# Kernel tuning notes

Hardware: AMD Instinct MI355X
Metric: run time of the kernel (lower is better)

The kernel has to match this reference:

```python
import jax, jax.numpy as jnp
import numpy as np

B, D, H, Wd = 256, 15, 63, 126  # batch, depth, lat, lon
K = 5                            # kernel == stride (reduce_resolution)
PD, PH, PW = 0, 1, 2             # ZeroPadding3D sizes
OD, OH, OW = (D + 2 * PD) // K, (H + 2 * PH) // K, (Wd + 2 * PW) // K  # 3,13,26


def setup_inputs() -> dict:
    key = jax.random.key(0)
    k1, k2, k3, k4 = jax.random.split(key, 4)
    x = jax.random.normal(k1, (B, D, H, Wd, 1), dtype=jnp.float32)
    # binary ocean mask: 1 = ocean (kept), 0 = land (removed)
    land = (jax.random.uniform(k2, (D, H, Wd, 1)) > 0.25).astype(jnp.float32)
    # positive cell volumes
    volumes = jax.random.uniform(k3, (D, H, Wd, 1), dtype=jnp.float32) + 0.5
    # per-location (non-shared) locally-connected weights
    W = jax.random.normal(k4, (OD, OH, OW, K, K, K, 1, 1), dtype=jnp.float32) / np.sqrt(K ** 3)
    b = jnp.zeros((OD, OH, OW, 1), dtype=jnp.float32)
    return {"x": x, "land": land, "volumes": volumes, "W": W, "b": b}


def reference(x, land, volumes, W, b):
    # LandValueRemoval3D (start): zero out land cells
    h = x * land
    # ZeroPadding3D((0,1,2))
    h = jnp.pad(h, ((0, 0), (0, 0), (PH, PH), (PW, PW), (0, 0)))
    # LocallyConnected3D, kernel==stride==5: non-overlapping blocks -> blocked einsum
    # (B, OD, K, OH, K, OW, K, C)
    hb = h.reshape(B, OD, K, OH, K, OW, K, 1)
    y = jnp.einsum('bipjqkrc,ijkpqrcf->bijkf', hb, W) + b  # per-location weights
    y = jax.nn.relu(y)
    # UpSampling3D((5,5,5))
    y = jnp.repeat(jnp.repeat(jnp.repeat(y, K, axis=1), K, axis=2), K, axis=3)
    # Cropping3D((0,1,2))
    y = y[:, :, PH:-PH, PW:-PW, :]
    # LandValueRemoval3D (end)
    y = y * land
    # MassConversation3D: rescale so total mass (x * volume) is conserved per sample
    mass_in = jnp.sum(x * volumes, axis=(1, 2, 3, 4), keepdims=True)
    mass_out = jnp.sum(y * volumes, axis=(1, 2, 3, 4), keepdims=True)
    return y * (mass_in / mass_out)
```

## Files before the change

### kernel.cpp

```cpp
#include <hip/hip_runtime.h>

#define BATCH 256
#define DD 15
#define HH 63
#define WW 126
#define OD 3
#define OH 13
#define OWI 26
#define SPAT (DD*HH*WW)
#define HWSZ (HH*WW)
#define NBLK (OD*OH*OWI)
#define IJB  (OH*OWI)
#define WEXP_D (65*130)
#define NWEXP (DD*WEXP_D)
#define NGRP 16

__global__ __launch_bounds__(256)
void prep_kernel(const float* __restrict__ W, const float* __restrict__ land,
                 const float* __restrict__ vols,
                 float* __restrict__ Wexp, float* __restrict__ lv,
                 unsigned short* __restrict__ tbl) {
    int idx = blockIdx.x * 256 + threadIdx.x;
    if (idx < NWEXP) {
        int d   = idx / WEXP_D;
        int rem = idx - d * WEXP_D;
        int hp1 = rem / 130;
        int wp  = rem - hp1 * 130;
        float val = 0.f;
        if (hp1 >= 1 && hp1 <= HH && wp >= 2 && wp < 128) {
            int i = d / 5, p = d - 5 * i;
            int h = hp1 - 1, w = wp - 2;
            int j = hp1 / 5, q = hp1 - 5 * j;
            int k = wp / 5,  r = wp - 5 * k;
            int blk = (i * OH + j) * OWI + k;
            val = W[blk * 125 + p * 25 + q * 5 + r] * land[(d * HH + h) * WW + w];
        }
        Wexp[idx] = val;
    } else if (idx < NWEXP + NBLK) {
        int blk = idx - NWEXP;
        int ij = blk / OWI, k = blk - ij * OWI;
        int i  = ij / OH,   j = ij - i * OH;
        float s = 0.f;
        for (int p = 0; p < 5; ++p) {
            int d = i * 5 + p;
            for (int q = 0; q < 5; ++q) {
                int h = j * 5 + q - 1;
                if ((unsigned)h >= (unsigned)HH) continue;
                int base = (d * HH + h) * WW;
                for (int r = 0; r < 5; ++r) {
                    int w = k * 5 + r - 2;
                    if ((unsigned)w < (unsigned)WW)
                        s += land[base + w] * vols[base + w];
                }
            }
        }
        lv[blk] = s;
    } else if (idx < NWEXP + NBLK + SPAT) {
        int r  = idx - NWEXP - NBLK;
        int d  = r / HWSZ;
        int r2 = r - d * HWSZ;
        int h  = r2 / WW;
        int w  = r2 - h * WW;
        tbl[r] = (unsigned short)(((d / 5) * OH + (h + 1) / 5) * OWI + (w + 2) / 5);
    }
}

__global__ __launch_bounds__(512)
void conv_kernel(const float* __restrict__ x, const float* __restrict__ vols,
                 const float* __restrict__ Wexp, const float* __restrict__ lv,
                 const float* __restrict__ bias, float* __restrict__ y_small,
                 double* __restrict__ mass_in, double* __restrict__ mass_out) {
    __shared__ float acc[NGRP * IJB];
    __shared__ float redmi[8];
    __shared__ float redmo[8];
    const int tid  = threadIdx.x;
    const int wv   = tid >> 6;
    const int lane = tid & 63;
    const int lg   = lane & 31;
    const int g    = wv * 2 + (lane >> 5);
    const int b    = blockIdx.x / OD;
    const int i    = blockIdx.x - b * OD;

    for (int t = tid; t < NGRP * IJB; t += 512) acc[t] = 0.f;
    __syncthreads();

    float mi = 0.f;
    if (lg < OWI) {
        const int wbase = 5 * lg - 2;
        const float* xb = x + (size_t)b * SPAT + i * 5 * HWSZ;
        const float* vb = vols + i * 5 * HWSZ;
        const float* wb = Wexp + i * 5 * WEXP_D;
        float* accw = acc + g * IJB + lg;
        for (int rr = g; rr < 5 * HH; rr += NGRP) {
            const int p = rr / HH;
            const int h = rr - p * HH;
            const float* xrow = xb + p * HWSZ + h * WW;
            const float* vrow = vb + p * HWSZ + h * WW;
            const float* wrow = wb + p * WEXP_D + (h + 1) * 130 + 5 * lg;
            float s = 0.f;
            #pragma unroll
            for (int r = 0; r < 5; ++r) {
                const int w = wbase + r;
                if ((unsigned)w < (unsigned)WW) {
                    const float xv = xrow[w];
                    s  = fmaf(xv, wrow[r], s);
                    mi = fmaf(xv, vrow[w], mi);
                }
            }
            accw[((h + 1) / 5) * OWI] += s;
        }
    }
    #pragma unroll
    for (int s2 = 32; s2; s2 >>= 1) mi += __shfl_down(mi, s2, 64);
    if (lane == 0) redmi[wv] = mi;
    __syncthreads();

    float mo = 0.f;
    if (tid < IJB) {
        float v = 0.f;
        #pragma unroll
        for (int w2 = 0; w2 < NGRP; ++w2) v += acc[w2 * IJB + tid];
        const int blk = i * IJB + tid;
        const float y = fmaxf(v + bias[blk], 0.f);
        y_small[(size_t)b * NBLK + blk] = y;
        mo = y * lv[blk];
    }
    #pragma unroll
    for (int s2 = 32; s2; s2 >>= 1) mo += __shfl_down(mo, s2, 64);
    if (lane == 0) redmo[wv] = mo;
    __syncthreads();
    if (tid == 0) {
        float tmi = 0.f, tmo = 0.f;
        #pragma unroll
        for (int w2 = 0; w2 < 8; ++w2) { tmi += redmi[w2]; tmo += redmo[w2]; }
        atomicAdd(mass_in  + b, (double)tmi);
        atomicAdd(mass_out + b, (double)tmo);
    }
}

__global__ void scale_kernel(const double* __restrict__ mi,
                             const double* __restrict__ mo,
                             float* __restrict__ s) {
    int t = threadIdx.x;
    if (t < BATCH) s[t] = (float)(mi[t] / mo[t]);
}

__global__ __launch_bounds__(256)
void out_kernel(const float* __restrict__ y, const unsigned short* __restrict__ tbl,
                const float* __restrict__ land, const float* __restrict__ scale,
                float4* __restrict__ out) {
    const unsigned PAIR4 = (2u * SPAT) / 4u;
    const unsigned CH    = 3721u;
    const unsigned b2    = blockIdx.x >> 4;
    const unsigned chunk = blockIdx.x & 15u;
    const unsigned begin = chunk * CH;
    const unsigned end   = (begin + CH < PAIR4) ? begin + CH : PAIR4;
    const float s0 = scale[2 * b2], s1 = scale[2 * b2 + 1];
    const float* y0 = y + (size_t)(2 * b2) * NBLK;
    const float* y1 = y0 + NBLK;
    const unsigned base4 = b2 * PAIR4;

    for (unsigned t = begin + threadIdx.x; t < end; t += 256) {
        const unsigned e0 = t * 4u;
        float o[4];
        #pragma unroll
        for (int up = 0; up < 2; ++up) {
            const unsigned e  = e0 + 2u * up;
            const unsigned bo = e >= (unsigned)SPAT;
            const unsigned r  = e - (bo ? (unsigned)SPAT : 0u);
            const unsigned tt = *reinterpret_cast<const unsigned*>(tbl + r);
            const float2   l2 = *reinterpret_cast<const float2*>(land + r);
            const float* yb = bo ? y1 : y0;
            const float  sc = bo ? s1 : s0;
            o[2 * up]     = yb[tt & 0xFFFFu] * l2.x * sc;
            o[2 * up + 1] = yb[tt >> 16]     * l2.y * sc;
        }
        out[base4 + t] = make_float4(o[0], o[1], o[2], o[3]);
    }
}

extern "C" void kernel_launch(void* const* d_in, const int* in_sizes, int n_in,
                              void* d_out, int out_size, void* d_ws, size_t ws_size,
                              hipStream_t stream) {
    const float* x    = (const float*)d_in[0];
    const float* land = (const float*)d_in[1];
    const float* vols = (const float*)d_in[2];
    const float* Wt   = (const float*)d_in[3];
    const float* bias = (const float*)d_in[4];

    char* ws = (char*)d_ws;
    double*         mass_in  = (double*)(ws);
    double*         mass_out = (double*)(ws + 2048);
    float*          scale    = (float*) (ws + 4096);
    float*          Wexp     = (float*) (ws + 5120);
    float*          lv       = (float*) (ws + 512120);
    unsigned short* tbl      = (unsigned short*)(ws + 516176);
    float*          y_small  = (float*) (ws + 754320);

    hipMemsetAsync(ws, 0, 4096, stream);

    prep_kernel<<<(NWEXP + NBLK + SPAT + 255) / 256, 256, 0, stream>>>(
        Wt, land, vols, Wexp, lv, tbl);

    conv_kernel<<<BATCH * OD, 512, 0, stream>>>(
        x, vols, Wexp, lv, bias, y_small, mass_in, mass_out);

    scale_kernel<<<1, 256, 0, stream>>>(mass_in, mass_out, scale);

    out_kernel<<<128 * 16, 256, 0, stream>>>(
        y_small, tbl, land, scale, (float4*)d_out);
}
```

Before: 340.4 us.

## Unroll conv rows by four, stage scaled y in LDS, use nontemporal output stores

```diff
diff --git a/kernel.cpp b/kernel.cpp
--- a/kernel.cpp
+++ b/kernel.cpp
@@ -14,6 +14,9 @@
 #define WEXP_D (65*130)
 #define NWEXP (DD*WEXP_D)
 #define NGRP 16
+#define NROWS (5*HH)
+
+typedef float f32x4 __attribute__((ext_vector_type(4)));
 
 __global__ __launch_bounds__(256)
 void prep_kernel(const float* __restrict__ W, const float* __restrict__ land,
@@ -84,32 +87,70 @@
     for (int t = tid; t < NGRP * IJB; t += 512) acc[t] = 0.f;
     __syncthreads();
 
-    float mi = 0.f;
+    float miv[4] = {0.f, 0.f, 0.f, 0.f};
     if (lg < OWI) {
         const int wbase = 5 * lg - 2;
         const float* xb = x + (size_t)b * SPAT + i * 5 * HWSZ;
         const float* vb = vols + i * 5 * HWSZ;
-        const float* wb = Wexp + i * 5 * WEXP_D;
-        float* accw = acc + g * IJB + lg;
-        for (int rr = g; rr < 5 * HH; rr += NGRP) {
+        const float* wb = Wexp + i * 5 * WEXP_D + 5 * lg;
+        float* accg = acc + g * IJB + lg;
+
+        const int start = 20 * g;
+        const int end   = (start + 20 < NROWS) ? start + 20 : NROWS;
+
+        int rr = start;
+        for (; rr + 3 < end; rr += 4) {
+            float s[4];
+            #pragma unroll
+            for (int u = 0; u < 4; ++u) {
+                const int row = rr + u;
+                const int p = row / HH;
+                const int h = row - p * HH;
+                const float* xrow = xb + p * HWSZ + h * WW;
+                const float* vrow = vb + p * HWSZ + h * WW;
+                const float* wrow = wb + p * WEXP_D + (h + 1) * 130;
+                float sv = 0.f;
+                float mv = miv[u];
+                #pragma unroll
+                for (int r = 0; r < 5; ++r) {
+                    const int w = wbase + r;
+                    if ((unsigned)w < (unsigned)WW) {
+                        const float xv = xrow[w];
+                        sv = fmaf(xv, wrow[r], sv);
+                        mv = fmaf(xv, vrow[w], mv);
+                    }
+                }
+                miv[u] = mv;
+                s[u] = sv;
+            }
+            #pragma unroll
+            for (int u = 0; u < 4; ++u) {
+                const int row = rr + u;
+                const int p = row / HH;
+                const int h = row - p * HH;
+                accg[((h + 1) / 5) * OWI] += s[u];
+            }
+        }
+        for (; rr < end; ++rr) {
             const int p = rr / HH;
             const int h = rr - p * HH;
             const float* xrow = xb + p * HWSZ + h * WW;
             const float* vrow = vb + p * HWSZ + h * WW;
-            const float* wrow = wb + p * WEXP_D + (h + 1) * 130 + 5 * lg;
-            float s = 0.f;
+            const float* wrow = wb + p * WEXP_D + (h + 1) * 130;
+            float sv = 0.f;
             #pragma unroll
             for (int r = 0; r < 5; ++r) {
                 const int w = wbase + r;
                 if ((unsigned)w < (unsigned)WW) {
                     const float xv = xrow[w];
-                    s  = fmaf(xv, wrow[r], s);
-                    mi = fmaf(xv, vrow[w], mi);
+                    sv     = fmaf(xv, wrow[r], sv);
+                    miv[0] = fmaf(xv, vrow[w], miv[0]);
                 }
             }
-            accw[((h + 1) / 5) * OWI] += s;
-        }
-    }
+            accg[((h + 1) / 5) * OWI] += sv;
+        }
+    }
+    float mi = (miv[0] + miv[1]) + (miv[2] + miv[3]);
     #pragma unroll
     for (int s2 = 32; s2; s2 >>= 1) mi += __shfl_down(mi, s2, 64);
     if (lane == 0) redmi[wv] = mi;
@@ -148,7 +189,8 @@
 __global__ __launch_bounds__(256)
 void out_kernel(const float* __restrict__ y, const unsigned short* __restrict__ tbl,
                 const float* __restrict__ land, const float* __restrict__ scale,
-                float4* __restrict__ out) {
+                f32x4* __restrict__ out) {
+    __shared__ float ylds[2 * NBLK];
     const unsigned PAIR4 = (2u * SPAT) / 4u;
     const unsigned CH    = 3721u;
     const unsigned b2    = blockIdx.x >> 4;
@@ -156,10 +198,12 @@
     const unsigned begin = chunk * CH;
     const unsigned end   = (begin + CH < PAIR4) ? begin + CH : PAIR4;
     const float s0 = scale[2 * b2], s1 = scale[2 * b2 + 1];
-    const float* y0 = y + (size_t)(2 * b2) * NBLK;
-    const float* y1 = y0 + NBLK;
+    const float* yb = y + (size_t)(2 * b2) * NBLK;
+    for (int t = threadIdx.x; t < 2 * NBLK; t += 256)
+        ylds[t] = yb[t] * (t < NBLK ? s0 : s1);
+    __syncthreads();
+
     const unsigned base4 = b2 * PAIR4;
-
     for (unsigned t = begin + threadIdx.x; t < end; t += 256) {
         const unsigned e0 = t * 4u;
         float o[4];
@@ -170,12 +214,13 @@
             const unsigned r  = e - (bo ? (unsigned)SPAT : 0u);
             const unsigned tt = *reinterpret_cast<const unsigned*>(tbl + r);
             const float2   l2 = *reinterpret_cast<const float2*>(land + r);
-            const float* yb = bo ? y1 : y0;
-            const float  sc = bo ? s1 : s0;
-            o[2 * up]     = yb[tt & 0xFFFFu] * l2.x * sc;
-            o[2 * up + 1] = yb[tt >> 16]     * l2.y * sc;
-        }
-        out[base4 + t] = make_float4(o[0], o[1], o[2], o[3]);
+            const unsigned yo = bo ? (unsigned)NBLK : 0u;
+            o[2 * up]     = ylds[yo + (tt & 0xFFFFu)] * l2.x;
+            o[2 * up + 1] = ylds[yo + (tt >> 16)]     * l2.y;
+        }
+        f32x4 v;
+        v.x = o[0]; v.y = o[1]; v.z = o[2]; v.w = o[3];
+        __builtin_nontemporal_store(v, &out[base4 + t]);
     }
 }
 
@@ -197,7 +242,7 @@
     unsigned short* tbl      = (unsigned short*)(ws + 516176);
     float*          y_small  = (float*) (ws + 754320);
 
-    hipMemsetAsync(ws, 0, 4096, stream);
+    (void)hipMemsetAsync(ws, 0, 4096, stream);
 
     prep_kernel<<<(NWEXP + NBLK + SPAT + 255) / 256, 256, 0, stream>>>(
         Wt, land, vols, Wexp, lv, tbl);
@@ -208,5 +253,5 @@
     scale_kernel<<<1, 256, 0, stream>>>(mass_in, mass_out, scale);
 
     out_kernel<<<128 * 16, 256, 0, stream>>>(
-        y_small, tbl, land, scale, (float4*)d_out);
-}
+        y_small, tbl, land, scale, (f32x4*)d_out);
+}
```

Measured after the change: 356.2 us. +4.6%, slower.
